# Performance work log

Measured on AMD Instinct MI355X. Metric: run time of the kernel, lower is better.

The kernel has to match this reference:

```python
import jax, jax.numpy as jnp
import numpy as np

B, N, H = 8, 1024, 768
NUM_HEADS = 12
HEAD_DIM = H // NUM_HEADS
EDGE_VOCAB = 32
SCALE = 1.0 / np.sqrt(HEAD_DIM)


def setup_inputs() -> dict:
    key = jax.random.key(0)
    ks = jax.random.split(key, 12)
    s = 0.02
    return {
        "x": jax.random.normal(ks[0], (B, N, H), dtype=jnp.float32),
        "E": jax.random.randint(ks[1], (B, N, N), 0, EDGE_VOCAB, dtype=jnp.int64),
        "M": jax.random.randint(ks[2], (B, N), 0, 2, dtype=jnp.int32),
        "Wq": jax.random.normal(ks[3], (H, H), dtype=jnp.float32) * s,
        "bq": jnp.zeros((H,), dtype=jnp.float32),
        "Wk": jax.random.normal(ks[4], (H, H), dtype=jnp.float32) * s,
        "bk": jnp.zeros((H,), dtype=jnp.float32),
        "Wv": jax.random.normal(ks[5], (H, H), dtype=jnp.float32) * s,
        "bv": jnp.zeros((H,), dtype=jnp.float32),
        "Wo": jax.random.normal(ks[6], (H, H), dtype=jnp.float32) * s,
        "bo": jnp.zeros((H,), dtype=jnp.float32),
        "edge_emb": jax.random.normal(ks[7], (EDGE_VOCAB, NUM_HEADS), dtype=jnp.float32) * s,
    }


def reference(x, E, M, Wq, bq, Wk, bk, Wv, bv, Wo, bo, edge_emb):
    b, n, h = x.shape
    nh, hd = NUM_HEADS, HEAD_DIM
    # projections (y = x @ W + b, W stored as (in, out))
    Q = (x @ Wq + bq).reshape(b, n, nh, hd).transpose(0, 2, 1, 3)  # (B,h,N,d)
    K = (x @ Wk + bk).reshape(b, n, nh, hd).transpose(0, 2, 1, 3)
    V = (x @ Wv + bv).reshape(b, n, nh, hd).transpose(0, 2, 1, 3)
    scores = jnp.einsum('bhnd,bhmd->bhnm', Q, K) * SCALE
    # edge bias: (B,N,N) tokens -> (B,N,N,h) -> (B,h,N,N)
    bias = edge_emb[E].transpose(0, 3, 1, 2)
    scores = scores + bias
    # dual masking: mask key positions (M[j]==0) and query positions (M[i]==0)
    valid = (M[:, None, None, :] != 0) & (M[:, None, :, None] != 0)  # (B,1,N,N)
    scores = jnp.where(valid, scores, -1e9)
    attn = jax.nn.softmax(scores, axis=-1)
    out = jnp.einsum('bhnm,bhmd->bhnd', attn, V)
    out = out.transpose(0, 2, 1, 3).reshape(b, n, h)
    return out @ Wo + bo
```

## Files before the change

kernel.cpp:

```cpp
#include <hip/hip_runtime.h>
#include <stdint.h>

#define DEV __device__ __forceinline__

typedef __attribute__((ext_vector_type(8))) short bf16x8;
typedef __attribute__((ext_vector_type(4))) float f32x4;
typedef __attribute__((ext_vector_type(16))) float f32x16;

DEV unsigned short f2bf(float f) {
  union { float f; uint32_t u; } v; v.f = f;
  uint32_t r = v.u + 0x7fffu + ((v.u >> 16) & 1u);
  return (unsigned short)(r >> 16);
}

DEV void lds_load16(void* dst, const void* src) {
  __builtin_amdgcn_global_load_lds(
      (const __attribute__((address_space(1))) unsigned int*)src,
      (__attribute__((address_space(3))) unsigned int*)dst, 16, 0, 0);
}


__global__ void conv_x_k(const float* __restrict__ x, unsigned short* __restrict__ o) {
  const int i = blockIdx.x * 256 + threadIdx.x;
  const float4 v = ((const float4*)x)[i];
  ushort4 u;
  u.x = f2bf(v.x); u.y = f2bf(v.y); u.z = f2bf(v.z); u.w = f2bf(v.w);
  ((ushort4*)o)[i] = u;
}

__global__ void conv_E_k(const int* __restrict__ E, const int* __restrict__ Mm,
                         uint8_t* __restrict__ E8L) {
  const int tid = blockIdx.x * 256 + threadIdx.x;
  const int k4 = tid & 255;
  const int q = (tid >> 8) & 1023;
  const int b = tid >> 18;
  const uint4 e = ((const uint4*)E)[tid];
  const int mq = Mm[b * 1024 + q];
  const int4 mk = *(const int4*)&Mm[b * 1024 + k4 * 4];
  uint32_t r;
  {
    const uint32_t b0 = (mq && mk.x) ? (e.x & 31u) : 32u;
    const uint32_t b1 = (mq && mk.y) ? (e.y & 31u) : 32u;
    const uint32_t b2 = (mq && mk.z) ? (e.z & 31u) : 32u;
    const uint32_t b3 = (mq && mk.w) ? (e.w & 31u) : 32u;
    r = b0 | (b1 << 8) | (b2 << 16) | (b3 << 24);
  }
  const int kt = k4 >> 4;
  const int k4t = k4 & 15;
  const int h = k4t & 1, c = (k4t >> 1) & 3, a = k4t >> 3;
  const int lane = (h << 5) | (q & 31);
  const int qw = q >> 5;
  const int j = a * 4 + c;
  const size_t rec = ((((size_t)b * 32 + qw) * 16 + kt) * 64 + lane) * 32 + j * 4;
  *(uint32_t*)(E8L + rec) = r;
}

__global__ void transp_w_k(const float* __restrict__ Wq, const float* __restrict__ Wk,
                           const float* __restrict__ Wv, const float* __restrict__ Wo,
                           unsigned short* __restrict__ wtqkv, unsigned short* __restrict__ wot) {
  __shared__ float tile[64][65];
  const int z = blockIdx.z;
  const float* W = (z == 0) ? Wq : (z == 1) ? Wk : (z == 2) ? Wv : Wo;
  unsigned short* D = (z < 3) ? wtqkv + (size_t)z * 768 * 768 : wot;
  const int k0 = blockIdx.x * 64;
  const int c0 = blockIdx.y * 64;
  const int t = threadIdx.x;
#pragma unroll
  for (int i = 0; i < 4; ++i) {
    const int idx = i * 256 + t;
    const int r = idx >> 4;
    const int cq = (idx & 15) * 4;
    const float4 v = *(const float4*)&W[(k0 + r) * 768 + c0 + cq];
    tile[r][cq] = v.x; tile[r][cq + 1] = v.y; tile[r][cq + 2] = v.z; tile[r][cq + 3] = v.w;
  }
  __syncthreads();
#pragma unroll
  for (int i = 0; i < 4; ++i) {
    const int idx = i * 256 + t;
    const int c = idx >> 4;
    const int kq = (idx & 15) * 4;
    ushort4 u;
    u.x = f2bf(tile[kq][c]);     u.y = f2bf(tile[kq + 1][c]);
    u.z = f2bf(tile[kq + 2][c]); u.w = f2bf(tile[kq + 3][c]);
    *(ushort4*)&D[(c0 + c) * 768 + k0 + kq] = u;
  }
}

template <int MODE>
__global__ __launch_bounds__(256, 2)
void gemm_bt(const unsigned short* __restrict__ A, const unsigned short* __restrict__ Bt,
             const float* __restrict__ b0, const float* __restrict__ b1, const float* __restrict__ b2,
             unsigned short* __restrict__ Qb, unsigned short* __restrict__ Kb,
             unsigned short* __restrict__ Vt, float* __restrict__ Fo) {
  __shared__ __attribute__((aligned(16))) unsigned short lds[2][16384];
  const int t = threadIdx.x;
  const int lane = t & 63;
  const int wid = t >> 6;

  const int id = blockIdx.x;
  const int xcd = id & 7;
  const int q = id >> 3;
  const int bx = xcd * 8 + (q & 7);
  const int by = q >> 3;
  const int m0 = bx * 128;
  const int n0 = by * 128;
  const int wm = (wid >> 1) * 64;
  const int wn = (wid & 1) * 64;

  const f32x4 Z4 = {0.f, 0.f, 0.f, 0.f};
  f32x4 acc[4][4];
#pragma unroll
  for (int m = 0; m < 4; ++m)
#pragma unroll
    for (int n = 0; n < 4; ++n) acc[m][n] = Z4;

  const unsigned short* gA0 = A + (size_t)m0 * 768;
  const unsigned short* gB0 = Bt + (size_t)n0 * 768;

  auto stage = [&](int buf, int kt) {
#pragma unroll
    for (int j = 0; j < 4; ++j) {
      const int u = j * 256 + t;
      const int kc = u >> 7;
      const int row = u & 127;
      const int dst = (j * 256 + wid * 64) * 8;
      lds_load16(&lds[buf][dst], gA0 + row * 768 + kt * 64 + kc * 8);
      lds_load16(&lds[buf][8192 + dst], gB0 + row * 768 + kt * 64 + kc * 8);
    }
  };

  stage(0, 0);
  int cur = 0;
  const int g = lane >> 4;
  const int c15 = lane & 15;

  for (int kt = 0; kt < 12; ++kt) {
    __syncthreads();
    if (kt + 1 < 12) stage(cur ^ 1, kt + 1);
#pragma unroll
    for (int kh = 0; kh < 2; ++kh) {
      const int kc = kh * 4 + g;
      bf16x8 av[4], bvv[4];
#pragma unroll
      for (int m = 0; m < 4; ++m)
        av[m] = *(const bf16x8*)&lds[cur][kc * 1024 + (wm + m * 16 + c15) * 8];
#pragma unroll
      for (int n = 0; n < 4; ++n)
        bvv[n] = *(const bf16x8*)&lds[cur][8192 + kc * 1024 + (wn + n * 16 + c15) * 8];
      __builtin_amdgcn_s_setprio(1);
#pragma unroll
      for (int m = 0; m < 4; ++m)
#pragma unroll
        for (int n = 0; n < 4; ++n)
          acc[m][n] = __builtin_amdgcn_mfma_f32_16x16x32_bf16(av[m], bvv[n], acc[m][n], 0, 0, 0);
      __builtin_amdgcn_s_setprio(0);
    }
    cur ^= 1;
  }

  if (MODE == 1) {
#pragma unroll
    for (int n = 0; n < 4; ++n) {
      const int col = n0 + wn + n * 16 + c15;
      const float bval = b0[col];
#pragma unroll
      for (int m = 0; m < 4; ++m) {
        const int r0 = m0 + wm + m * 16 + g * 4;
#pragma unroll
        for (int r = 0; r < 4; ++r) Fo[(r0 + r) * 768 + col] = acc[m][n][r] + bval;
      }
    }
  } else {
    const int mat = by / 6;
    const float* bsel = (mat == 0) ? b0 : (mat == 1) ? b1 : b2;
    unsigned short* qk = (mat == 0) ? Qb : Kb;
#pragma unroll
    for (int n = 0; n < 4; ++n) {
      const int cw = (by % 6) * 128 + wn + n * 16 + c15;
      const int hh = cw >> 6, dd = cw & 63;
      const float bval = bsel[cw];
#pragma unroll
      for (int m = 0; m < 4; ++m) {
        const int r0 = m0 + wm + m * 16 + g * 4;
        const int bb = r0 >> 10;
        const int nn = r0 & 1023;
        if (mat < 2) {
          unsigned short* dst = qk + ((bb * 12 + hh) * 1024 + nn) * 64 + dd;
#pragma unroll
          for (int r = 0; r < 4; ++r) dst[r * 64] = f2bf(acc[m][n][r] + bval);
        } else {
          ushort4 w;
          w.x = f2bf(acc[m][n][0] + bval);
          w.y = f2bf(acc[m][n][1] + bval);
          w.z = f2bf(acc[m][n][2] + bval);
          w.w = f2bf(acc[m][n][3] + bval);
          *(ushort4*)&Vt[((bb * 12 + hh) * 64 + dd) * 1024 + nn] = w;
        }
      }
    }
  }
}

__global__ __launch_bounds__(256, 3)
void attn_fused(const unsigned short* __restrict__ Qb, const unsigned short* __restrict__ Kb,
                const unsigned short* __restrict__ Vt, const uint8_t* __restrict__ E8L,
                const float* __restrict__ emb, unsigned short* __restrict__ AO) {
  __shared__ __attribute__((aligned(16))) unsigned short Ks[2][4096];
  __shared__ __attribute__((aligned(16))) unsigned short Vs[2][4096];
  __shared__ float ttab[33];
  __shared__ float red[4][32];

  const int t = threadIdx.x;
  const int lane = t & 63;
  const int wid = t >> 6;
  const int l31 = lane & 31;
  const int hl = lane >> 5;

  const int id = blockIdx.x;
  const int sw = (id & 7) * 96 + (id >> 3);
  const int b = sw / 96;
  const int rem = sw - b * 96;
  const int h = rem >> 3;
  const int qb = rem & 7;
  const int bh = b * 12 + h;
  const int qw = qb * 4 + wid;
  const int q0 = qw * 32;

  if (t < 33) ttab[t] = (t < 32) ? emb[t * 12 + h] * 1.44269504f : -1e30f;

  bf16x8 qf[4];
  {
    const unsigned short* qp = Qb + ((size_t)bh * 1024 + q0 + l31) * 64 + hl * 8;
#pragma unroll
    for (int dc = 0; dc < 4; ++dc) qf[dc] = *(const bf16x8*)(qp + dc * 16);
  }

  auto stageKV = [&](int buf, int kt) {
#pragma unroll
    for (int i = 0; i < 2; ++i) {
      const int c = i * 256 + t;
      const int row = c >> 3, c16 = c & 7;
      const int sc = (c16 ^ (row & 7)) * 8;
      lds_load16(&Ks[buf][i * 2048 + wid * 512],
                 Kb + ((size_t)bh * 1024 + kt * 64 + row) * 64 + sc);
      lds_load16(&Vs[buf][i * 2048 + wid * 512],
                 Vt + ((size_t)bh * 64 + row) * 1024 + kt * 64 + sc);
    }
  };

  const uint8_t* ebase = E8L + (((size_t)(b * 32 + qw)) * 16 * 64 + lane) * 32;

  stageKV(0, 0);
  uint4 e0 = *(const uint4*)(ebase);
  uint4 e1 = *(const uint4*)(ebase + 16);

  const f32x16 Z16 = {0.f};
  f32x16 oacc0 = Z16, oacc1 = Z16;
  float m = -3.0e38f, lsum = 0.f;
  int cur = 0;

  for (int kt = 0; kt < 16; ++kt) {
    __syncthreads();
    if (kt + 1 < 16) stageKV(cur ^ 1, kt + 1);
    uint4 en0, en1;
    if (kt + 1 < 16) {
      en0 = *(const uint4*)(ebase + (kt + 1) * 2048);
      en1 = *(const uint4*)(ebase + (kt + 1) * 2048 + 16);
    }

    f32x16 s0 = Z16, s1 = Z16;
    __builtin_amdgcn_s_setprio(1);
#pragma unroll
    for (int dc = 0; dc < 4; ++dc) {
      const int gch = (dc * 2 + hl);
      const bf16x8 a0 = *(const bf16x8*)((const char*)Ks[cur] +
                         l31 * 128 + ((gch ^ (l31 & 7)) << 4));
      const bf16x8 a1 = *(const bf16x8*)((const char*)Ks[cur] +
                         (32 + l31) * 128 + ((gch ^ ((32 + l31) & 7)) << 4));
      s0 = __builtin_amdgcn_mfma_f32_32x32x16_bf16(a0, qf[dc], s0, 0, 0, 0);
      s1 = __builtin_amdgcn_mfma_f32_32x32x16_bf16(a1, qf[dc], s1, 0, 0, 0);
    }
    __builtin_amdgcn_s_setprio(0);

    const uint32_t ed[8] = {e0.x, e0.y, e0.z, e0.w, e1.x, e1.y, e1.z, e1.w};
    float w0[16], w1[16];
#pragma unroll
    for (int r = 0; r < 16; ++r) {
      const uint32_t d0 = ed[r >> 2], d1 = ed[4 + (r >> 2)];
      const int sh = (r & 3) * 8;
      w0[r] = fmaf(s0[r], 0.18033688f, ttab[(d0 >> sh) & 0xffu]);
      w1[r] = fmaf(s1[r], 0.18033688f, ttab[(d1 >> sh) & 0xffu]);
    }

    float rm = fmaxf(w0[0], w1[0]);
#pragma unroll
    for (int r = 1; r < 16; ++r) rm = fmaxf(rm, fmaxf(w0[r], w1[r]));
    rm = fmaxf(rm, __shfl_xor(rm, 32, 64));

    if (__any(rm > m + 11.5415603f)) {
      const float mn = fmaxf(m, rm);
      const float scl = exp2f(m - mn);
      m = mn;
      lsum *= scl;
#pragma unroll
      for (int r = 0; r < 16; ++r) { oacc0[r] *= scl; oacc1[r] *= scl; }
    }

    float rs0 = 0.f, rs1 = 0.f, rs2 = 0.f, rs3 = 0.f;
#pragma unroll
    for (int r = 0; r < 16; ++r) {
      w0[r] = exp2f(w0[r] - m);
      w1[r] = exp2f(w1[r] - m);
    }
#pragma unroll
    for (int r = 0; r < 4; ++r) {
      rs0 += w0[r];  rs1 += w0[4 + r];
      rs2 += w0[8 + r]; rs3 += w0[12 + r];
      rs0 += w1[r];  rs1 += w1[4 + r];
      rs2 += w1[8 + r]; rs3 += w1[12 + r];
    }
    float rs = (rs0 + rs1) + (rs2 + rs3);
    rs += __shfl_xor(rs, 32, 64);
    lsum += rs;

    uint32_t wd0[8], wd1[8];
#pragma unroll
    for (int j = 0; j < 8; ++j) {
      asm("v_cvt_pk_bf16_f32 %0, %1, %2" : "=v"(wd0[j]) : "v"(w0[2 * j]), "v"(w0[2 * j + 1]));
      asm("v_cvt_pk_bf16_f32 %0, %1, %2" : "=v"(wd1[j]) : "v"(w1[2 * j]), "v"(w1[2 * j + 1]));
    }
#pragma unroll
    for (int cc = 0; cc < 2; ++cc) {
      asm volatile("v_permlane32_swap_b32 %0, %1" : "+v"(wd0[4 * cc]), "+v"(wd0[4 * cc + 2]));
      asm volatile("v_permlane32_swap_b32 %0, %1" : "+v"(wd0[4 * cc + 1]), "+v"(wd0[4 * cc + 3]));
      asm volatile("v_permlane32_swap_b32 %0, %1" : "+v"(wd1[4 * cc]), "+v"(wd1[4 * cc + 2]));
      asm volatile("v_permlane32_swap_b32 %0, %1" : "+v"(wd1[4 * cc + 1]), "+v"(wd1[4 * cc + 3]));
    }

    __builtin_amdgcn_s_setprio(1);
#pragma unroll
    for (int kb = 0; kb < 4; ++kb) {
      union { uint32_t u[4]; bf16x8 v; } fu;
      const uint32_t* wds = (kb < 2) ? wd0 : wd1;
      const int cc = kb & 1;
      fu.u[0] = wds[4 * cc];     fu.u[1] = wds[4 * cc + 1];
      fu.u[2] = wds[4 * cc + 2]; fu.u[3] = wds[4 * cc + 3];
      const int gch = kb * 2 + hl;
      const bf16x8 v0 = *(const bf16x8*)((const char*)Vs[cur] +
                         l31 * 128 + ((gch ^ (l31 & 7)) << 4));
      const bf16x8 v1 = *(const bf16x8*)((const char*)Vs[cur] +
                         (32 + l31) * 128 + ((gch ^ ((32 + l31) & 7)) << 4));
      oacc0 = __builtin_amdgcn_mfma_f32_32x32x16_bf16(fu.v, v0, oacc0, 0, 0, 0);
      oacc1 = __builtin_amdgcn_mfma_f32_32x32x16_bf16(fu.v, v1, oacc1, 0, 0, 0);
    }
    __builtin_amdgcn_s_setprio(0);

    e0 = en0; e1 = en1;
    cur ^= 1;
  }

  red[wid][l31] = 1.0f / lsum;
  __syncthreads();
  unsigned short* aob = AO + ((size_t)b * 1024 + q0) * 768 + h * 64;
#pragma unroll
  for (int j = 0; j < 4; ++j) {
    const f32x4 lv = *(const f32x4*)&red[wid][8 * j + 4 * hl];
#pragma unroll
    for (int rr = 0; rr < 4; ++rr) {
      const int rowq = rr + 8 * j + 4 * hl;
      const int reg = 4 * j + rr;
      aob[rowq * 768 + l31]      = f2bf(oacc0[reg] * lv[rr]);
      aob[rowq * 768 + 32 + l31] = f2bf(oacc1[reg] * lv[rr]);
    }
  }
}


extern "C" void kernel_launch(void* const* d_in, const int* in_sizes, int n_in,
                              void* d_out, int out_size, void* d_ws, size_t ws_size,
                              hipStream_t stream) {
  (void)in_sizes; (void)n_in; (void)out_size; (void)ws_size;
  const float* x = (const float*)d_in[0];
  const int* E = (const int*)d_in[1];
  const int* Mm = (const int*)d_in[2];
  const float* Wq = (const float*)d_in[3];
  const float* bq = (const float*)d_in[4];
  const float* Wk = (const float*)d_in[5];
  const float* bk = (const float*)d_in[6];
  const float* Wv = (const float*)d_in[7];
  const float* bv = (const float*)d_in[8];
  const float* Wo = (const float*)d_in[9];
  const float* bo = (const float*)d_in[10];
  const float* emb = (const float*)d_in[11];
  float* out = (float*)d_out;

  char* w = (char*)d_ws;
  unsigned short* x16 = (unsigned short*)w;
  unsigned short* AO = x16;
  w += (size_t)8192 * 768 * 2;
  unsigned short* wtqkv = (unsigned short*)w; w += (size_t)2304 * 768 * 2;
  unsigned short* wot = (unsigned short*)w;   w += (size_t)768 * 768 * 2;
  unsigned short* Qb = (unsigned short*)w;    w += (size_t)8 * 12 * 1024 * 64 * 2;
  unsigned short* Kb = (unsigned short*)w;    w += (size_t)8 * 12 * 1024 * 64 * 2;
  unsigned short* Vt = (unsigned short*)w;    w += (size_t)8 * 12 * 64 * 1024 * 2;
  uint8_t* E8L = (uint8_t*)w;                 w += (size_t)8 * 1024 * 1024;

  conv_x_k<<<6144, 256, 0, stream>>>(x, x16);
  conv_E_k<<<8192, 256, 0, stream>>>(E, Mm, E8L);
  transp_w_k<<<dim3(12, 12, 4), 256, 0, stream>>>(Wq, Wk, Wv, Wo, wtqkv, wot);
  gemm_bt<0><<<1152, 256, 0, stream>>>(x16, wtqkv, bq, bk, bv, Qb, Kb, Vt, nullptr);
  attn_fused<<<768, 256, 0, stream>>>(Qb, Kb, Vt, E8L, emb, AO);
  gemm_bt<1><<<384, 256, 0, stream>>>(AO, wot, bo, nullptr, nullptr,
                                      nullptr, nullptr, nullptr, out);
}
```

Measured before the change: 186.4 us.

## Triple-buffer GEMM K-loop with smaller K tiles and manual waitcnt barriers

Restructures the projection GEMM mainloop from a double-buffered K=64 tile into a triple-buffered K=32 tile pipeline, prefetching two stages ahead. It uses explicit vmcnt/lgkmcnt waits and raw s_barrier so loads stay in flight across iterations. LDS per block shrinks from 64KB to 48KB and launch bounds rise to 3 blocks per CU, aiming to hide global-load latency and raise occupancy. It risks more barriers per K step and correctness depending on exact vmcnt counts.

```diff
diff --git a/kernel.cpp b/kernel.cpp
--- a/kernel.cpp
+++ b/kernel.cpp
@@ -87,25 +87,27 @@
 }
 
 template <int MODE>
-__global__ __launch_bounds__(256, 2)
+__global__ __launch_bounds__(256, 3)
 void gemm_bt(const unsigned short* __restrict__ A, const unsigned short* __restrict__ Bt,
              const float* __restrict__ b0, const float* __restrict__ b1, const float* __restrict__ b2,
              unsigned short* __restrict__ Qb, unsigned short* __restrict__ Kb,
              unsigned short* __restrict__ Vt, float* __restrict__ Fo) {
-  __shared__ __attribute__((aligned(16))) unsigned short lds[2][16384];
+  __shared__ __attribute__((aligned(16))) unsigned short lds[3][8192];
   const int t = threadIdx.x;
   const int lane = t & 63;
   const int wid = t >> 6;
 
   const int id = blockIdx.x;
   const int xcd = id & 7;
-  const int q = id >> 3;
-  const int bx = xcd * 8 + (q & 7);
-  const int by = q >> 3;
+  const int qq = id >> 3;
+  const int bx = xcd * 8 + (qq & 7);
+  const int by = qq >> 3;
   const int m0 = bx * 128;
   const int n0 = by * 128;
   const int wm = (wid >> 1) * 64;
   const int wn = (wid & 1) * 64;
+  const int g = lane >> 4;
+  const int c15 = lane & 15;
 
   const f32x4 Z4 = {0.f, 0.f, 0.f, 0.f};
   f32x4 acc[4][4];
@@ -119,44 +121,55 @@
 
   auto stage = [&](int buf, int kt) {
 #pragma unroll
-    for (int j = 0; j < 4; ++j) {
+    for (int j = 0; j < 2; ++j) {
       const int u = j * 256 + t;
       const int kc = u >> 7;
       const int row = u & 127;
-      const int dst = (j * 256 + wid * 64) * 8;
-      lds_load16(&lds[buf][dst], gA0 + row * 768 + kt * 64 + kc * 8);
-      lds_load16(&lds[buf][8192 + dst], gB0 + row * 768 + kt * 64 + kc * 8);
+      unsigned short* dA = &lds[buf][(j * 256 + wid * 64) * 8];
+      const unsigned short* sA = gA0 + row * 768 + kt * 32 + kc * 8;
+      const unsigned short* sB = gB0 + row * 768 + kt * 32 + kc * 8;
+      lds_load16(dA, sA);
+      lds_load16(dA + 4096, sB);
     }
   };
 
+  const int a_off = g * 1024 + (wm + c15) * 8;
+  const int b_off = 4096 + g * 1024 + (wn + c15) * 8;
+  auto compute = [&](int buf) {
+    bf16x8 av[4], bvv[4];
+#pragma unroll
+    for (int m = 0; m < 4; ++m) av[m] = *(const bf16x8*)&lds[buf][a_off + m * 128];
+#pragma unroll
+    for (int n = 0; n < 4; ++n) bvv[n] = *(const bf16x8*)&lds[buf][b_off + n * 128];
+    __builtin_amdgcn_s_setprio(1);
+#pragma unroll
+    for (int m = 0; m < 4; ++m)
+#pragma unroll
+      for (int n = 0; n < 4; ++n)
+        acc[m][n] = __builtin_amdgcn_mfma_f32_16x16x32_bf16(av[m], bvv[n], acc[m][n], 0, 0, 0);
+    __builtin_amdgcn_s_setprio(0);
+  };
+
   stage(0, 0);
-  int cur = 0;
-  const int g = lane >> 4;
-  const int c15 = lane & 15;
-
-  for (int kt = 0; kt < 12; ++kt) {
-    __syncthreads();
-    if (kt + 1 < 12) stage(cur ^ 1, kt + 1);
-#pragma unroll
-    for (int kh = 0; kh < 2; ++kh) {
-      const int kc = kh * 4 + g;
-      bf16x8 av[4], bvv[4];
-#pragma unroll
-      for (int m = 0; m < 4; ++m)
-        av[m] = *(const bf16x8*)&lds[cur][kc * 1024 + (wm + m * 16 + c15) * 8];
-#pragma unroll
-      for (int n = 0; n < 4; ++n)
-        bvv[n] = *(const bf16x8*)&lds[cur][8192 + kc * 1024 + (wn + n * 16 + c15) * 8];
-      __builtin_amdgcn_s_setprio(1);
-#pragma unroll
-      for (int m = 0; m < 4; ++m)
-#pragma unroll
-        for (int n = 0; n < 4; ++n)
-          acc[m][n] = __builtin_amdgcn_mfma_f32_16x16x32_bf16(av[m], bvv[n], acc[m][n], 0, 0, 0);
-      __builtin_amdgcn_s_setprio(0);
-    }
-    cur ^= 1;
-  }
+  stage(1, 1);
+  for (int kt = 0; kt < 22; ++kt) {
+    stage((kt + 2) % 3, kt + 2);
+    asm volatile("s_waitcnt vmcnt(8)" ::: "memory");
+    __builtin_amdgcn_sched_barrier(0);
+    asm volatile("s_barrier" ::: "memory");
+    compute(kt % 3);
+    asm volatile("s_waitcnt lgkmcnt(0)" ::: "memory");
+    __builtin_amdgcn_sched_barrier(0);
+    asm volatile("s_barrier" ::: "memory");
+  }
+  asm volatile("s_waitcnt vmcnt(4)" ::: "memory");
+  __builtin_amdgcn_sched_barrier(0);
+  asm volatile("s_barrier" ::: "memory");
+  compute(22 % 3);
+  asm volatile("s_waitcnt vmcnt(0)" ::: "memory");
+  __builtin_amdgcn_sched_barrier(0);
+  asm volatile("s_barrier" ::: "memory");
+  compute(23 % 3);
 
   if (MODE == 1) {
 #pragma unroll
```

Result: no change. 184.4 us (-1.0%).
